# Performance work log

Hardware: AMD Instinct MI355X
Metric: run time of the kernel (lower is better)

## Reference

```python
import jax, jax.numpy as jnp
import numpy as np

B, S, D, H, Dh = 2, 1024, 2048, 16, 128
EPS = 1e-6


def setup_inputs() -> dict:
    key = jax.random.key(0)
    ks = jax.random.split(key, 8)
    hidden_states = jax.random.normal(ks[0], (B, S, D), jnp.float32)
    def qweight(k):
        return jax.random.randint(k, (D, D), -127, 128, dtype=jnp.int32)
    wq, wk, wv, wo = qweight(ks[1]), qweight(ks[2]), qweight(ks[3]), qweight(ks[4])
    def scale(k):
        # per-output-channel dequant scale ~ O(1/(127*sqrt(D)))
        return jax.random.uniform(k, (D,), jnp.float32, 0.5, 1.5) / (127.0 * np.sqrt(D))
    wq_s, wk_s, wv_s, wo_s = scale(ks[5]), scale(ks[6]), scale(ks[7]), scale(jax.random.fold_in(key, 99))
    qn_w = jnp.ones((D,), jnp.float32)
    kn_w = jnp.ones((D,), jnp.float32)
    # RoPE tables (rotate-half convention): [S, Dh]
    pos = jnp.arange(S, dtype=jnp.float32)
    inv_freq = 1.0 / (10000.0 ** (jnp.arange(0, Dh, 2, dtype=jnp.float32) / Dh))
    freqs = pos[:, None] * inv_freq[None, :]              # [S, Dh/2]
    cos = jnp.concatenate([jnp.cos(freqs)] * 2, axis=-1)  # [S, Dh]
    sin = jnp.concatenate([jnp.sin(freqs)] * 2, axis=-1)
    lengths = jnp.array([S, 3 * S // 4], dtype=jnp.int32)
    return dict(hidden_states=hidden_states, wq_s=wq_s, wk_s=wk_s, wv_s=wv_s,
                wo_s=wo_s, qn_w=qn_w, kn_w=kn_w, cos=cos, sin=sin,
                wq=wq, wk=wk, wv=wv, wo=wo, lengths=lengths)


def _q8_linear(x, w_int, scale):
    # Q8Linear: int8 weight [out,in] dequantized by per-output-channel scale
    w = w_int.astype(jnp.float32) * scale[:, None]
    return jnp.einsum('bsd,od->bso', x, w)


def _rms_norm(x, w):
    var = jnp.mean(jnp.square(x), axis=-1, keepdims=True)
    return x * jax.lax.rsqrt(var + EPS) * w


def _apply_rope(x, cos, sin):
    # x: [B,S,D] -> per-head rotate-half RoPE -> [B,S,D]
    xh = x.reshape(B, S, H, Dh)
    x1, x2 = jnp.split(xh, 2, axis=-1)
    rot = jnp.concatenate([-x2, x1], axis=-1)
    out = xh * cos[None, :, None, :] + rot * sin[None, :, None, :]
    return out.reshape(B, S, D)


def reference(hidden_states, wq_s, wk_s, wv_s, wo_s, qn_w, kn_w, cos, sin,
              wq, wk, wv, wo, lengths):
    q = _rms_norm(_q8_linear(hidden_states, wq, wq_s), qn_w)
    k = _rms_norm(_q8_linear(hidden_states, wk, wk_s), kn_w)
    v = _q8_linear(hidden_states, wv, wv_s)
    q = _apply_rope(q, cos, sin)
    k = _apply_rope(k, cos, sin)
    # [B,S,D] -> [B,H,S,Dh]
    q = q.reshape(B, S, H, Dh).transpose(0, 2, 1, 3)
    k = k.reshape(B, S, H, Dh).transpose(0, 2, 1, 3)
    v = v.reshape(B, S, H, Dh).transpose(0, 2, 1, 3)
    # length mask -> additive bias [B,1,1,S]
    positions = jnp.arange(S)
    valid = positions[None, :] < lengths[:, None]
    bias = jnp.where(valid, 0.0, -jnp.inf).astype(jnp.float32)[:, None, None, :]
    scores = jnp.einsum('bhqd,bhkd->bhqk', q, k) / np.sqrt(Dh) + bias
    probs = jax.nn.softmax(scores, axis=-1)
    attn = jnp.einsum('bhqk,bhkd->bhqd', probs, v)
    attn = attn.transpose(0, 2, 1, 3).reshape(B, S, D)
    out = _q8_linear(attn, wo, wo_s)
    return out
```

## Files before the change

### kernel.cpp

```cpp
#include <hip/hip_runtime.h>
#include <stdint.h>

typedef __bf16 bf16;
typedef bf16 bf16x8 __attribute__((ext_vector_type(8)));
typedef bf16 bf16x4 __attribute__((ext_vector_type(4)));
typedef float f32x4 __attribute__((ext_vector_type(4)));

#define B_   2
#define S_   1024
#define D_   2048
#define H_   16
#define DH_  128
#define M_   (B_*S_)
#define EPSF 1e-6f

__device__ __forceinline__ void gload_lds16(const void* g, void* l) {
    __builtin_amdgcn_global_load_lds(
        (const __attribute__((address_space(1))) void*)g,
        (__attribute__((address_space(3))) void*)l,
        16, 0, 0);
}

struct ConvArgs {
    const void* s[5];
    bf16* d[5];
};

__global__ __launch_bounds__(256) void conv_all(ConvArgs a, int n) {
    const int z = blockIdx.y;
    const int i = (blockIdx.x * 256 + threadIdx.x) * 8;
    if (i + 8 > n) return;
    bf16x8 o;
    if (z == 0) {
        const float* src = (const float*)a.s[0];
        float4 v0 = *(const float4*)(src + i);
        float4 v1 = *(const float4*)(src + i + 4);
        o[0] = (bf16)v0.x; o[1] = (bf16)v0.y; o[2] = (bf16)v0.z; o[3] = (bf16)v0.w;
        o[4] = (bf16)v1.x; o[5] = (bf16)v1.y; o[6] = (bf16)v1.z; o[7] = (bf16)v1.w;
    } else {
        const int* src = (const int*)a.s[z];
        int4 v0 = *(const int4*)(src + i);
        int4 v1 = *(const int4*)(src + i + 4);
        o[0] = (bf16)(float)v0.x; o[1] = (bf16)(float)v0.y;
        o[2] = (bf16)(float)v0.z; o[3] = (bf16)(float)v0.w;
        o[4] = (bf16)(float)v1.x; o[5] = (bf16)(float)v1.y;
        o[6] = (bf16)(float)v1.z; o[7] = (bf16)(float)v1.w;
    }
    *(bf16x8*)(a.d[z] + i) = o;
}

struct GemmArgs {
    const bf16* W[3];
    const float* Sc[3];
    void* O[3];
    int mode[3];
};

__global__ __launch_bounds__(512, 2) void gemm8p(const bf16* __restrict__ A, GemmArgs args) {
    __shared__ char lds[131072];
    constexpr int NT = D_ / 64;

    const int z = blockIdx.z;
    const bf16* __restrict__ Wz = args.W[z];
    const float* __restrict__ Sc = args.Sc[z];
    const int mode = args.mode[z];
    const int t = threadIdx.x;
    const int w = t >> 6, l = t & 63;
    const int wr = w >> 2, wc = w & 3;
    const int m0 = blockIdx.y * 256, n0 = blockIdx.x * 256;
    const int hi = l >> 4, lo = l & 15;

    const int r8 = l >> 3;
    const int ce = ((l & 7) ^ (r8 & 7)) * 8;
    const bf16* Ag = A  + (size_t)(m0 + w * 8 + r8) * D_ + ce;
    const bf16* Bg = Wz + (size_t)(n0 + w * 8 + r8) * D_ + ce;

    auto stage = [&](int kt, int q) {
        if (kt >= NT) return;
        const bf16* g = (q < 2 ? Ag : Bg) + (size_t)((q & 1) * 128) * D_ + (size_t)kt * 64;
        char* d = lds + ((kt & 1) ? 65536 : 0) + q * 16384 + w * 1024;
        gload_lds16((const void*)g, (void*)d);
        gload_lds16((const void*)(g + (size_t)64 * D_), (void*)(d + 8192));
    };

    f32x4 acc[8][4] = {};

    stage(0, 0); stage(0, 1); stage(0, 2); stage(0, 3);
    stage(1, 2); stage(1, 0);
    asm volatile("s_waitcnt vmcnt(4)" ::: "memory");
    asm volatile("s_barrier" ::: "memory");

    for (int kt = 0; kt < NT; ++kt) {
        const char* Pb = lds + ((kt & 1) ? 65536 : 0);
        const char* As = Pb;
        const char* Bs = Pb + 32768;
        bf16x8 a[4][2], b01[2][2], b23[2][2];

        auto rdA = [&](int mi, int kk) -> bf16x8 {
            int row = wr * 128 + mi * 16 + lo;
            return *(const bf16x8*)(As + row * 128 + ((kk * 64 + hi * 16) ^ ((row & 7) << 4)));
        };
        auto rdB = [&](int ni, int kk) -> bf16x8 {
            int row = wc * 64 + ni * 16 + lo;
            return *(const bf16x8*)(Bs + row * 128 + ((kk * 64 + hi * 16) ^ ((row & 7) << 4)));
        };

#pragma unroll
        for (int mi = 0; mi < 4; ++mi) { a[mi][0] = rdA(mi, 0); a[mi][1] = rdA(mi, 1); }
#pragma unroll
        for (int ni = 0; ni < 2; ++ni) { b01[ni][0] = rdB(ni, 0); b01[ni][1] = rdB(ni, 1); }
        stage(kt + 1, 1);
        asm volatile("s_barrier" ::: "memory");
        asm volatile("s_waitcnt lgkmcnt(0)" ::: "memory");
        __builtin_amdgcn_sched_barrier(0);
        __builtin_amdgcn_s_setprio(1);
#pragma unroll
        for (int mi = 0; mi < 4; ++mi)
#pragma unroll
            for (int ni = 0; ni < 2; ++ni)
#pragma unroll
                for (int kk = 0; kk < 2; ++kk)
                    acc[mi][ni] = __builtin_amdgcn_mfma_f32_16x16x32_bf16(a[mi][kk], b01[ni][kk], acc[mi][ni], 0, 0, 0);
        __builtin_amdgcn_s_setprio(0);
        asm volatile("s_barrier" ::: "memory");

#pragma unroll
        for (int ni = 0; ni < 2; ++ni) { b23[ni][0] = rdB(2 + ni, 0); b23[ni][1] = rdB(2 + ni, 1); }
        stage(kt + 1, 3);
        asm volatile("s_barrier" ::: "memory");
        asm volatile("s_waitcnt lgkmcnt(0)" ::: "memory");
        __builtin_amdgcn_sched_barrier(0);
        __builtin_amdgcn_s_setprio(1);
#pragma unroll
        for (int mi = 0; mi < 4; ++mi)
#pragma unroll
            for (int ni = 0; ni < 2; ++ni)
#pragma unroll
                for (int kk = 0; kk < 2; ++kk)
                    acc[mi][2 + ni] = __builtin_amdgcn_mfma_f32_16x16x32_bf16(a[mi][kk], b23[ni][kk], acc[mi][2 + ni], 0, 0, 0);
        __builtin_amdgcn_s_setprio(0);
        asm volatile("s_barrier" ::: "memory");

#pragma unroll
        for (int mi = 0; mi < 4; ++mi) { a[mi][0] = rdA(4 + mi, 0); a[mi][1] = rdA(4 + mi, 1); }
        stage(kt + 2, 2);
        asm volatile("s_barrier" ::: "memory");
        asm volatile("s_waitcnt lgkmcnt(0)" ::: "memory");
        __builtin_amdgcn_sched_barrier(0);
        __builtin_amdgcn_s_setprio(1);
#pragma unroll
        for (int mi = 0; mi < 4; ++mi)
#pragma unroll
            for (int ni = 0; ni < 2; ++ni)
#pragma unroll
                for (int kk = 0; kk < 2; ++kk)
                    acc[4 + mi][2 + ni] = __builtin_amdgcn_mfma_f32_16x16x32_bf16(a[mi][kk], b23[ni][kk], acc[4 + mi][2 + ni], 0, 0, 0);
        __builtin_amdgcn_s_setprio(0);
        asm volatile("s_barrier" ::: "memory");

        stage(kt + 2, 0);
        asm volatile("s_barrier" ::: "memory");
        __builtin_amdgcn_sched_barrier(0);
        __builtin_amdgcn_s_setprio(1);
#pragma unroll
        for (int mi = 0; mi < 4; ++mi)
#pragma unroll
            for (int ni = 0; ni < 2; ++ni)
#pragma unroll
                for (int kk = 0; kk < 2; ++kk)
                    acc[4 + mi][ni] = __builtin_amdgcn_mfma_f32_16x16x32_bf16(a[mi][kk], b01[ni][kk], acc[4 + mi][ni], 0, 0, 0);
        __builtin_amdgcn_s_setprio(0);
        if (kt < NT - 2) asm volatile("s_waitcnt vmcnt(4)" ::: "memory");
        else             asm volatile("s_waitcnt vmcnt(0)" ::: "memory");
        asm volatile("s_barrier" ::: "memory");
    }

#pragma unroll
    for (int ni = 0; ni < 4; ++ni) {
        const int n = n0 + wc * 64 + ni * 16 + lo;
        const float scv = Sc[n];
#pragma unroll
        for (int mi = 0; mi < 8; ++mi) {
            const int mb = m0 + wr * 128 + mi * 16 + hi * 4;
            if (mode == 1) {
                bf16x4 pk;
#pragma unroll
                for (int r = 0; r < 4; ++r) pk[r] = (bf16)(acc[mi][ni][r] * scv);
                const int bb = mb >> 10, s = mb & 1023, hh = n >> 7, dh = n & 127;
                *(bf16x4*)(((bf16*)args.O[z]) + (((size_t)(bb * H_ + hh)) * DH_ + dh) * S_ + s) = pk;
            } else {
#pragma unroll
                for (int r = 0; r < 4; ++r)
                    ((bf16*)args.O[z])[(size_t)(mb + r) * D_ + n] = (bf16)(acc[mi][ni][r] * scv);
            }
        }
    }
}

__global__ __launch_bounds__(256, 2) void gemmO(const bf16* __restrict__ A, const bf16* __restrict__ W,
                                                const float* __restrict__ Sc, float* __restrict__ O) {
    __shared__ char lds[65536];
    constexpr int NT = D_ / 64;
    const int t = threadIdx.x;
    const int w = t >> 6, l = t & 63;
    const int wr = w >> 1, wc = w & 1;
    const int m0 = blockIdx.y * 128, n0 = blockIdx.x * 128;
    const int hi = l >> 4, lo = l & 15;

    const int r8 = l >> 3;
    const int ce = ((l & 7) ^ (r8 & 7)) * 8;
    const bf16* Ag = A + (size_t)(m0 + w * 8 + r8) * D_ + ce;
    const bf16* Bg = W + (size_t)(n0 + w * 8 + r8) * D_ + ce;

    auto stage = [&](int kt) {
        char* d = lds + (kt & 1) * 32768 + w * 1024;
        const bf16* ga = Ag + (size_t)kt * 64;
        const bf16* gb = Bg + (size_t)kt * 64;
#pragma unroll
        for (int j = 0; j < 4; ++j) {
            gload_lds16((const void*)(ga + (size_t)j * 32 * D_), (void*)(d + j * 4096));
            gload_lds16((const void*)(gb + (size_t)j * 32 * D_), (void*)(d + 16384 + j * 4096));
        }
    };

    f32x4 acc[4][4] = {};
    stage(0);
    for (int kt = 0; kt < NT; ++kt) {
        const char* cur = lds + (kt & 1) * 32768;
        if (kt + 1 < NT) {
            stage(kt + 1);
            asm volatile("s_waitcnt vmcnt(8)" ::: "memory");
        } else {
            asm volatile("s_waitcnt vmcnt(0)" ::: "memory");
        }
        asm volatile("s_barrier" ::: "memory");

        bf16x8 a[4][2], b[4][2];
#pragma unroll
        for (int mi = 0; mi < 4; ++mi)
#pragma unroll
            for (int kk = 0; kk < 2; ++kk) {
                int row = wr * 64 + mi * 16 + lo;
                a[mi][kk] = *(const bf16x8*)(cur + row * 128 + ((kk * 64 + hi * 16) ^ ((row & 7) << 4)));
            }
#pragma unroll
        for (int ni = 0; ni < 4; ++ni)
#pragma unroll
            for (int kk = 0; kk < 2; ++kk) {
                int row = wc * 64 + ni * 16 + lo;
                b[ni][kk] = *(const bf16x8*)(cur + 16384 + row * 128 + ((kk * 64 + hi * 16) ^ ((row & 7) << 4)));
            }
        __builtin_amdgcn_s_setprio(1);
#pragma unroll
        for (int mi = 0; mi < 4; ++mi)
#pragma unroll
            for (int ni = 0; ni < 4; ++ni)
#pragma unroll
                for (int kk = 0; kk < 2; ++kk)
                    acc[mi][ni] = __builtin_amdgcn_mfma_f32_16x16x32_bf16(a[mi][kk], b[ni][kk], acc[mi][ni], 0, 0, 0);
        __builtin_amdgcn_s_setprio(0);
        asm volatile("s_barrier" ::: "memory");
    }

#pragma unroll
    for (int ni = 0; ni < 4; ++ni) {
        const int n = n0 + wc * 64 + ni * 16 + lo;
        const float scv = Sc[n];
#pragma unroll
        for (int mi = 0; mi < 4; ++mi) {
            const int mb = m0 + wr * 64 + mi * 16 + hi * 4;
#pragma unroll
            for (int r = 0; r < 4; ++r)
                O[(size_t)(mb + r) * D_ + n] = acc[mi][ni][r] * scv;
        }
    }
}

__global__ __launch_bounds__(256) void rope_norm(const bf16* __restrict__ qr, const bf16* __restrict__ kr,
                                                 const float* __restrict__ qn, const float* __restrict__ kn,
                                                 const float* __restrict__ cosT, const float* __restrict__ sinT,
                                                 bf16* __restrict__ qOut, bf16* __restrict__ kOut) {
    const int which = blockIdx.z;
    const bf16* src = which ? kr : qr;
    const float* nw = which ? kn : qn;
    bf16* dst = which ? kOut : qOut;
    const int row = blockIdx.x;
    const int b = row >> 10, s = row & 1023;
    const int t = threadIdx.x;
    __shared__ float xs[D_];
    __shared__ float red[4];

    bf16x8 v = *(const bf16x8*)(src + (size_t)row * D_ + t * 8);
    float x[8]; float ss = 0.f;
#pragma unroll
    for (int j = 0; j < 8; ++j) { x[j] = (float)v[j]; ss += x[j] * x[j]; xs[t * 8 + j] = x[j]; }
#pragma unroll
    for (int msk = 32; msk; msk >>= 1) ss += __shfl_xor(ss, msk, 64);
    if ((t & 63) == 0) red[t >> 6] = ss;
    __syncthreads();
    const float inv = rsqrtf((red[0] + red[1] + red[2] + red[3]) / (float)D_ + EPSF);

    const int h = t >> 4;
    const int dh0 = (t & 15) * 8;
    bf16x8 o;
#pragma unroll
    for (int j = 0; j < 8; ++j) {
        int dd = dh0 + j;
        int d = h * 128 + dd;
        int pd = (dd < 64) ? d + 64 : d - 64;
        float xn = x[j] * inv * nw[d];
        float xp = xs[pd] * inv * nw[pd];
        float rot = (dd < 64) ? -xp : xp;
        o[j] = (bf16)(xn * cosT[s * DH_ + dd] + rot * sinT[s * DH_ + dd]);
    }
    *(bf16x8*)(dst + (((size_t)(b * H_ + h)) * S_ + s) * DH_ + dh0) = o;
}

__global__ __launch_bounds__(256) void flash(const bf16* __restrict__ Q, const bf16* __restrict__ Kb,
                                             const bf16* __restrict__ VTb, const int* __restrict__ lengths,
                                             bf16* __restrict__ Out) {
    __shared__ bf16 Qs[64 * 128];
    __shared__ bf16 Ks[64 * 128];
    __shared__ bf16 Vt[128 * 64];
    __shared__ bf16 Ps[4][16 * 64];
    const int t = threadIdx.x, w = t >> 6, l = t & 63;
    const int bh = blockIdx.y;
    const int b = bh >> 4;
    const int q0 = blockIdx.x * 64;
    const int L = lengths[b];
    const size_t base = (size_t)bh * S_ * DH_;
    const size_t vbase = (size_t)bh * DH_ * S_;
    const int hi = l >> 4, lo = l & 15;
    const int swz = (lo & 7) << 3;

    {
        const bf16* src = Q + base + (size_t)q0 * DH_;
#pragma unroll
        for (int i = 0; i < 4; ++i) {
            int r = (w * 4 + i) * 4 + (l >> 4);
            int sb = ((l & 15) * 16) ^ ((r & 7) << 4);
            gload_lds16((const void*)(src + (size_t)r * DH_ + (sb >> 1)), (void*)(Qs + (w * 4 + i) * 512));
        }
    }

    f32x4 O[8] = {};
    float mrow[4], lrow[4];
#pragma unroll
    for (int r = 0; r < 4; ++r) { mrow[r] = -1e30f; lrow[r] = 0.f; }
    const int nt = (L + 63) >> 6;
    const float sscale = 0.08838834764831843f;

    for (int kt = 0; kt < nt; ++kt) {
        const int k0 = kt * 64;
        __syncthreads();
        {
            const bf16* ksrc = Kb + base + (size_t)k0 * DH_;
#pragma unroll
            for (int i = 0; i < 4; ++i) {
                int r = (w * 4 + i) * 4 + (l >> 4);
                int sb = ((l & 15) * 16) ^ ((r & 7) << 4);
                gload_lds16((const void*)(ksrc + (size_t)r * DH_ + (sb >> 1)), (void*)(Ks + (w * 4 + i) * 512));
            }
        }
        {
            const bf16* vsrc = VTb + vbase + k0;
#pragma unroll
            for (int i = 0; i < 4; ++i) {
                int d = (w * 4 + i) * 8 + (l >> 3);
                int sb = ((l & 7) * 16) ^ ((d & 7) << 4);
                gload_lds16((const void*)(vsrc + (size_t)d * S_ + (sb >> 1)), (void*)(Vt + (w * 4 + i) * 512));
            }
        }
        __syncthreads();

        f32x4 sc[4] = {};
#pragma unroll
        for (int kk = 0; kk < 4; ++kk) {
            const int ko = kk * 32 + hi * 8;
            bf16x8 aq = *(const bf16x8*)(Qs + (w * 16 + lo) * 128 + (ko ^ swz));
#pragma unroll
            for (int ni = 0; ni < 4; ++ni) {
                bf16x8 bk = *(const bf16x8*)(Ks + (ni * 16 + lo) * 128 + (ko ^ swz));
                sc[ni] = __builtin_amdgcn_mfma_f32_16x16x32_bf16(aq, bk, sc[ni], 0, 0, 0);
            }
        }

        float p[4][4];
#pragma unroll
        for (int r = 0; r < 4; ++r) {
            float sv[4]; float vmax = -1e30f;
#pragma unroll
            for (int ni = 0; ni < 4; ++ni) {
                int kg = k0 + ni * 16 + lo;
                float vv = sc[ni][r] * sscale;
                if (kg >= L) vv = -1e30f;
                sv[ni] = vv;
                vmax = fmaxf(vmax, vv);
            }
#pragma unroll
            for (int msk = 1; msk < 16; msk <<= 1) vmax = fmaxf(vmax, __shfl_xor(vmax, msk, 64));
            float mnew = fmaxf(mrow[r], vmax);
            float corr = __expf(mrow[r] - mnew);
            float rs = 0.f;
#pragma unroll
            for (int ni = 0; ni < 4; ++ni) { float pv = __expf(sv[ni] - mnew); p[r][ni] = pv; rs += pv; }
#pragma unroll
            for (int msk = 1; msk < 16; msk <<= 1) rs += __shfl_xor(rs, msk, 64);
            lrow[r] = lrow[r] * corr + rs;
            mrow[r] = mnew;
#pragma unroll
            for (int di = 0; di < 8; ++di) O[di][r] *= corr;
        }

#pragma unroll
        for (int r = 0; r < 4; ++r) {
            int prow = hi * 4 + r;
#pragma unroll
            for (int ni = 0; ni < 4; ++ni)
                Ps[w][prow * 64 + (((ni * 16 + lo)) ^ ((prow & 7) << 3))] = (bf16)p[r][ni];
        }

#pragma unroll
        for (int kk = 0; kk < 2; ++kk) {
            const int ko = kk * 32 + hi * 8;
            bf16x8 ap = *(const bf16x8*)(&Ps[w][lo * 64 + (ko ^ swz)]);
#pragma unroll
            for (int di = 0; di < 8; ++di) {
                bf16x8 bv = *(const bf16x8*)(Vt + (di * 16 + lo) * 64 + (ko ^ swz));
                O[di] = __builtin_amdgcn_mfma_f32_16x16x32_bf16(ap, bv, O[di], 0, 0, 0);
            }
        }
    }

    const int h = bh & 15;
#pragma unroll
    for (int r = 0; r < 4; ++r) {
        float invl = 1.0f / lrow[r];
        int qrow = q0 + w * 16 + hi * 4 + r;
        bf16* orow = Out + (size_t)(b * S_ + qrow) * D_ + h * DH_;
#pragma unroll
        for (int di = 0; di < 8; ++di)
            orow[di * 16 + lo] = (bf16)(O[di][r] * invl);
    }
}

extern "C" void kernel_launch(void* const* d_in, const int* in_sizes, int n_in,
                              void* d_out, int out_size, void* d_ws, size_t ws_size,
                              hipStream_t stream) {
    const float* x    = (const float*)d_in[0];
    const float* wq_s = (const float*)d_in[1];
    const float* wk_s = (const float*)d_in[2];
    const float* wv_s = (const float*)d_in[3];
    const float* wo_s = (const float*)d_in[4];
    const float* qn   = (const float*)d_in[5];
    const float* kn   = (const float*)d_in[6];
    const float* cosT = (const float*)d_in[7];
    const float* sinT = (const float*)d_in[8];
    const int* wq = (const int*)d_in[9];
    const int* wk = (const int*)d_in[10];
    const int* wv = (const int*)d_in[11];
    const int* wo = (const int*)d_in[12];
    const int* lengths = (const int*)d_in[13];
    float* out = (float*)d_out;

    char* ws = (char*)d_ws;
    const size_t SLOT = (size_t)M_ * D_ * sizeof(bf16);
    bf16* xb   = (bf16*)(ws);
    bf16* wqb  = (bf16*)(ws + 1 * SLOT);
    bf16* wkb  = (bf16*)(ws + 2 * SLOT);
    bf16* wvb  = (bf16*)(ws + 3 * SLOT);
    bf16* wob  = (bf16*)(ws + 4 * SLOT);
    bf16* qr   = (bf16*)(ws + 5 * SLOT);
    bf16* kr   = (bf16*)(ws + 6 * SLOT);
    bf16* qb2  = (bf16*)(ws + 7 * SLOT);
    bf16* kb2  = (bf16*)(ws + 8 * SLOT);
    bf16* vb2  = (bf16*)(ws + 9 * SLOT);
    bf16* attnb = qr;

    const int NW = D_ * D_;
    ConvArgs ca;
    ca.s[0] = x;  ca.d[0] = xb;
    ca.s[1] = wq; ca.d[1] = wqb;
    ca.s[2] = wk; ca.d[2] = wkb;
    ca.s[3] = wv; ca.d[3] = wvb;
    ca.s[4] = wo; ca.d[4] = wob;
    conv_all<<<dim3(NW / 2048, 5), dim3(256), 0, stream>>>(ca, NW);

    GemmArgs ga;
    ga.W[0] = wqb; ga.W[1] = wkb; ga.W[2] = wvb;
    ga.Sc[0] = wq_s; ga.Sc[1] = wk_s; ga.Sc[2] = wv_s;
    ga.O[0] = qr; ga.O[1] = kr; ga.O[2] = vb2;
    ga.mode[0] = 2; ga.mode[1] = 2; ga.mode[2] = 1;
    gemm8p<<<dim3(D_ / 256, M_ / 256, 3), dim3(512), 0, stream>>>(xb, ga);

    rope_norm<<<dim3(M_, 1, 2), dim3(256), 0, stream>>>(qr, kr, qn, kn, cosT, sinT, qb2, kb2);

    flash<<<dim3(S_ / 64, B_ * H_, 1), dim3(256), 0, stream>>>(qb2, kb2, vb2, lengths, attnb);

    gemmO<<<dim3(D_ / 128, M_ / 128), dim3(256), 0, stream>>>(attnb, wob, wo_s, out);
}
```

Measured before the change: 155.8 us.

## Fold wo conversion into QKV GEMM launch and widen flash tiles to 128 queries

The wo int32-to-bf16 conversion moves out of the conversion kernel into extra z=3 blocks of the QKV GEMM launch, so it runs alongside the GEMM work. The flash kernel now uses 512 threads and 128-query tiles, so each K/V tile loaded into LDS serves twice as many queries. It also raises wave priority around the MFMA sections with s_setprio. The trade-offs are a larger LDS footprint per flash block and only 256 flash blocks, which may lower occupancy and leave less parallelism to hide latency.

```diff
diff --git a/kernel.cpp b/kernel.cpp
--- a/kernel.cpp
+++ b/kernel.cpp
@@ -22,8 +22,8 @@
 }
 
 struct ConvArgs {
-    const void* s[5];
-    bf16* d[5];
+    const void* s[4];
+    bf16* d[4];
 };
 
 __global__ __launch_bounds__(256) void conv_all(ConvArgs a, int n) {
@@ -54,17 +54,38 @@
     const float* Sc[3];
     void* O[3];
     int mode[3];
+    const int* wo_src;
+    bf16* wo_dst;
 };
 
 __global__ __launch_bounds__(512, 2) void gemm8p(const bf16* __restrict__ A, GemmArgs args) {
     __shared__ char lds[131072];
     constexpr int NT = D_ / 64;
-
     const int z = blockIdx.z;
+    const int t = threadIdx.x;
+
+    if (z == 3) {
+        const int flat = blockIdx.y * 8 + blockIdx.x;
+        const int* src = args.wo_src + (size_t)flat * 65536;
+        bf16* dst = args.wo_dst + (size_t)flat * 65536;
+#pragma unroll
+        for (int it = 0; it < 16; ++it) {
+            int off = it * 4096 + t * 8;
+            int4 v0 = *(const int4*)(src + off);
+            int4 v1 = *(const int4*)(src + off + 4);
+            bf16x8 o;
+            o[0] = (bf16)(float)v0.x; o[1] = (bf16)(float)v0.y;
+            o[2] = (bf16)(float)v0.z; o[3] = (bf16)(float)v0.w;
+            o[4] = (bf16)(float)v1.x; o[5] = (bf16)(float)v1.y;
+            o[6] = (bf16)(float)v1.z; o[7] = (bf16)(float)v1.w;
+            *(bf16x8*)(dst + off) = o;
+        }
+        return;
+    }
+
     const bf16* __restrict__ Wz = args.W[z];
     const float* __restrict__ Sc = args.Sc[z];
     const int mode = args.mode[z];
-    const int t = threadIdx.x;
     const int w = t >> 6, l = t & 63;
     const int wr = w >> 2, wc = w & 3;
     const int m0 = blockIdx.y * 256, n0 = blockIdx.x * 256;
@@ -316,17 +337,17 @@
     *(bf16x8*)(dst + (((size_t)(b * H_ + h)) * S_ + s) * DH_ + dh0) = o;
 }
 
-__global__ __launch_bounds__(256) void flash(const bf16* __restrict__ Q, const bf16* __restrict__ Kb,
+__global__ __launch_bounds__(512) void flash(const bf16* __restrict__ Q, const bf16* __restrict__ Kb,
                                              const bf16* __restrict__ VTb, const int* __restrict__ lengths,
                                              bf16* __restrict__ Out) {
-    __shared__ bf16 Qs[64 * 128];
+    __shared__ bf16 Qs[128 * 128];
     __shared__ bf16 Ks[64 * 128];
     __shared__ bf16 Vt[128 * 64];
-    __shared__ bf16 Ps[4][16 * 64];
+    __shared__ bf16 Ps[8][16 * 64];
     const int t = threadIdx.x, w = t >> 6, l = t & 63;
     const int bh = blockIdx.y;
     const int b = bh >> 4;
-    const int q0 = blockIdx.x * 64;
+    const int q0 = blockIdx.x * 128;
     const int L = lengths[b];
     const size_t base = (size_t)bh * S_ * DH_;
     const size_t vbase = (size_t)bh * DH_ * S_;
@@ -337,9 +358,10 @@
         const bf16* src = Q + base + (size_t)q0 * DH_;
 #pragma unroll
         for (int i = 0; i < 4; ++i) {
-            int r = (w * 4 + i) * 4 + (l >> 4);
+            int pb = w * 4 + i;
+            int r = pb * 4 + (l >> 4);
             int sb = ((l & 15) * 16) ^ ((r & 7) << 4);
-            gload_lds16((const void*)(src + (size_t)r * DH_ + (sb >> 1)), (void*)(Qs + (w * 4 + i) * 512));
+            gload_lds16((const void*)(src + (size_t)r * DH_ + (sb >> 1)), (void*)(Qs + pb * 512));
         }
     }
 
@@ -356,24 +378,27 @@
         {
             const bf16* ksrc = Kb + base + (size_t)k0 * DH_;
 #pragma unroll
-            for (int i = 0; i < 4; ++i) {
-                int r = (w * 4 + i) * 4 + (l >> 4);
+            for (int i = 0; i < 2; ++i) {
+                int pb = w * 2 + i;
+                int r = pb * 4 + (l >> 4);
                 int sb = ((l & 15) * 16) ^ ((r & 7) << 4);
-                gload_lds16((const void*)(ksrc + (size_t)r * DH_ + (sb >> 1)), (void*)(Ks + (w * 4 + i) * 512));
+                gload_lds16((const void*)(ksrc + (size_t)r * DH_ + (sb >> 1)), (void*)(Ks + pb * 512));
             }
         }
         {
             const bf16* vsrc = VTb + vbase + k0;
 #pragma unroll
-            for (int i = 0; i < 4; ++i) {
-                int d = (w * 4 + i) * 8 + (l >> 3);
+            for (int i = 0; i < 2; ++i) {
+                int pb = w * 2 + i;
+                int d = pb * 8 + (l >> 3);
                 int sb = ((l & 7) * 16) ^ ((d & 7) << 4);
-                gload_lds16((const void*)(vsrc + (size_t)d * S_ + (sb >> 1)), (void*)(Vt + (w * 4 + i) * 512));
+                gload_lds16((const void*)(vsrc + (size_t)d * S_ + (sb >> 1)), (void*)(Vt + pb * 512));
             }
         }
         __syncthreads();
 
         f32x4 sc[4] = {};
+        __builtin_amdgcn_s_setprio(1);
 #pragma unroll
         for (int kk = 0; kk < 4; ++kk) {
             const int ko = kk * 32 + hi * 8;
@@ -384,6 +409,7 @@
                 sc[ni] = __builtin_amdgcn_mfma_f32_16x16x32_bf16(aq, bk, sc[ni], 0, 0, 0);
             }
         }
+        __builtin_amdgcn_s_setprio(0);
 
         float p[4][4];
 #pragma unroll
@@ -420,6 +446,7 @@
                 Ps[w][prow * 64 + (((ni * 16 + lo)) ^ ((prow & 7) << 3))] = (bf16)p[r][ni];
         }
 
+        __builtin_amdgcn_s_setprio(1);
 #pragma unroll
         for (int kk = 0; kk < 2; ++kk) {
             const int ko = kk * 32 + hi * 8;
@@ -430,6 +457,7 @@
                 O[di] = __builtin_amdgcn_mfma_f32_16x16x32_bf16(ap, bv, O[di], 0, 0, 0);
             }
         }
+        __builtin_amdgcn_s_setprio(0);
     }
 
     const int h = bh & 15;
@@ -483,19 +511,19 @@
     ca.s[1] = wq; ca.d[1] = wqb;
     ca.s[2] = wk; ca.d[2] = wkb;
     ca.s[3] = wv; ca.d[3] = wvb;
-    ca.s[4] = wo; ca.d[4] = wob;
-    conv_all<<<dim3(NW / 2048, 5), dim3(256), 0, stream>>>(ca, NW);
+    conv_all<<<dim3(NW / 2048, 4), dim3(256), 0, stream>>>(ca, NW);
 
     GemmArgs ga;
     ga.W[0] = wqb; ga.W[1] = wkb; ga.W[2] = wvb;
     ga.Sc[0] = wq_s; ga.Sc[1] = wk_s; ga.Sc[2] = wv_s;
     ga.O[0] = qr; ga.O[1] = kr; ga.O[2] = vb2;
     ga.mode[0] = 2; ga.mode[1] = 2; ga.mode[2] = 1;
-    gemm8p<<<dim3(D_ / 256, M_ / 256, 3), dim3(512), 0, stream>>>(xb, ga);
+    ga.wo_src = wo; ga.wo_dst = wob;
+    gemm8p<<<dim3(D_ / 256, M_ / 256, 4), dim3(512), 0, stream>>>(xb, ga);
 
     rope_norm<<<dim3(M_, 1, 2), dim3(256), 0, stream>>>(qr, kr, qn, kn, cosT, sinT, qb2, kb2);
 
-    flash<<<dim3(S_ / 64, B_ * H_, 1), dim3(256), 0, stream>>>(qb2, kb2, vb2, lengths, attnb);
+    flash<<<dim3(S_ / 128, B_ * H_, 1), dim3(512), 0, stream>>>(qb2, kb2, vb2, lengths, attnb);
 
     gemmO<<<dim3(D_ / 128, M_ / 128), dim3(256), 0, stream>>>(attnb, wob, wo_s, out);
 }
```

Measured after the change: 161.5 us. 1.04x slower.
